# Optimization experiments

Measured on AMD Instinct MI355X. Metric: run time of the kernel, lower is better.

## Reference

```python
import jax, jax.numpy as jnp
import numpy as np
from jax import lax

BN_EPS = 1e-5
C = 256


def _conv_bn_relu(x, w, gamma, beta, mean, var):
    # x: [B,C,H,W], w: [C,C,3,3]; VALID conv, stride 1, then inference BN + ReLU
    y = lax.conv_general_dilated(x, w, window_strides=(1, 1), padding='VALID',
                                 dimension_numbers=('NCHW', 'OIHW', 'NCHW'))
    scale = gamma * lax.rsqrt(var + BN_EPS)
    shift = beta - mean * scale
    y = y * scale[None, :, None, None] + shift[None, :, None, None]
    return jax.nn.relu(y)


def _xcorr_depthwise(search, kernel):
    # search: [B,C,Hs,Ws], kernel: [B,C,Hk,Wk]
    # per-(batch, channel) valid cross-correlation (groups = B*C in torch)
    c = search.shape[1]

    def one(s, k):  # s: [C,Hs,Ws], k: [C,Hk,Wk]
        return lax.conv_general_dilated(
            s[None], k[:, None], window_strides=(1, 1), padding='VALID',
            dimension_numbers=('NCHW', 'OIHW', 'NCHW'),
            feature_group_count=c)[0]

    return jax.vmap(one)(search, kernel)  # [B,C,Ho,Wo]


def setup_inputs() -> dict:
    key = jax.random.key(0)
    ks = jax.random.split(key, 8)
    B = 128
    kernel = jax.random.normal(ks[0], (B, C, 7, 7), dtype=jnp.float32)
    search = jax.random.normal(ks[1], (B, C, 31, 31), dtype=jnp.float32)
    std = np.sqrt(2.0 / (3 * 3 * C)).astype(np.float32)
    w_kernel = jax.random.normal(ks[2], (C, C, 3, 3), dtype=jnp.float32) * std
    w_search = jax.random.normal(ks[3], (C, C, 3, 3), dtype=jnp.float32) * std
    bn_k_gamma = jnp.ones((C,), jnp.float32)
    bn_k_beta = jnp.zeros((C,), jnp.float32)
    bn_k_mean = jax.random.normal(ks[4], (C,), dtype=jnp.float32) * 0.1
    bn_k_var = jax.random.uniform(ks[5], (C,), dtype=jnp.float32, minval=0.5, maxval=1.5)
    bn_s_gamma = jnp.ones((C,), jnp.float32)
    bn_s_beta = jnp.zeros((C,), jnp.float32)
    bn_s_mean = jax.random.normal(ks[6], (C,), dtype=jnp.float32) * 0.1
    bn_s_var = jax.random.uniform(ks[7], (C,), dtype=jnp.float32, minval=0.5, maxval=1.5)
    return dict(kernel=kernel, search=search,
                w_kernel=w_kernel, bn_k_gamma=bn_k_gamma, bn_k_beta=bn_k_beta,
                bn_k_mean=bn_k_mean, bn_k_var=bn_k_var,
                w_search=w_search, bn_s_gamma=bn_s_gamma, bn_s_beta=bn_s_beta,
                bn_s_mean=bn_s_mean, bn_s_var=bn_s_var)


def reference(kernel, search, w_kernel, bn_k_gamma, bn_k_beta, bn_k_mean, bn_k_var,
              w_search, bn_s_gamma, bn_s_beta, bn_s_mean, bn_s_var):
    k = _conv_bn_relu(kernel, w_kernel, bn_k_gamma, bn_k_beta, bn_k_mean, bn_k_var)  # [B,C,5,5]
    s = _conv_bn_relu(search, w_search, bn_s_gamma, bn_s_beta, bn_s_mean, bn_s_var)  # [B,C,29,29]
    return _xcorr_depthwise(s, k)  # [B,C,25,25]
```

## Files before the change

### kernel.cpp

```cpp
#include <hip/hip_runtime.h>
#include <hip/hip_bf16.h>

#define BN_EPS 1e-5f
constexpr int C = 256;

typedef __attribute__((ext_vector_type(8))) short bf16x8;
typedef __attribute__((ext_vector_type(4))) float f32x4;

static __device__ __forceinline__ unsigned short f2bf(float f) {
    __hip_bfloat16 h = __float2bfloat16(f);
    return *reinterpret_cast<unsigned short*>(&h);
}
static __device__ __forceinline__ float bf2f(unsigned short u) {
    unsigned int v = ((unsigned int)u) << 16;
    return __uint_as_float(v);
}
static __device__ __forceinline__ unsigned int pack_bf2(float a, float b) {
    return (unsigned int)f2bf(a) | ((unsigned int)f2bf(b) << 16);
}

__global__ __launch_bounds__(256) void wprep_both(
    const float* __restrict__ wk, const float* __restrict__ bkg, const float* __restrict__ bkv,
    unsigned short* __restrict__ wkt,
    const float* __restrict__ ws, const float* __restrict__ bsg, const float* __restrict__ bsv,
    unsigned short* __restrict__ wst)
{
    const int bid = blockIdx.x, t = threadIdx.x;
    const bool isk = bid < 256;
    const int n = isk ? bid : bid - 256;
    const float* w = isk ? wk : ws;
    const float* g = isk ? bkg : bsg;
    const float* v = isk ? bkv : bsv;
    unsigned short* wt = isk ? wkt : wst;
    const float scale = g[n] * rsqrtf(v[n] + BN_EPS);
    const float* wp = w + ((size_t)n * C + t) * 9;
#pragma unroll
    for (int k = 0; k < 9; ++k)
        wt[((size_t)k * C + n) * C + t] = f2bf(wp[k] * scale);
}

__global__ __launch_bounds__(512, 2) void mega_conv(
    const float* __restrict__ sin_,
    const float* __restrict__ kin,
    const unsigned short* __restrict__ wst,
    const unsigned short* __restrict__ wkt,
    const float* __restrict__ bsg, const float* __restrict__ bsb,
    const float* __restrict__ bsm, const float* __restrict__ bsv,
    const float* __restrict__ bkg, const float* __restrict__ bkb,
    const float* __restrict__ bkm, const float* __restrict__ bkv,
    unsigned short* __restrict__ sbuf,
    float* __restrict__ kbuf)
{
    constexpr int WOUT = 29, NPOS = 841;
    constexpr int BM = 224, MF = 7, NF = 4;
    constexpr int LDK = 36;
    constexpr int ROWS = 11;
    constexpr int APIX = ROWS * 31;
    constexpr int ABUF = APIX * LDK;
    constexpr int BBUF = 256 * LDK;
    constexpr int BIT = 2;

    __shared__ __align__(16) short s_a[2 * ABUF];
    __shared__ __align__(16) short s_b[4 * BBUF];

    const int bid = blockIdx.x;
    const int t = threadIdx.x;
    const int lane = t & 63, wave = t >> 6;
    const int lr = lane >> 4, lc = lane & 15;

    if (bid >= 512) {
        constexpr int KW = 7, KHW = 49, KWOUT = 5, KNPOS = 25;
        constexpr int KMF = 2, KNF = 2;
        const int kb = bid - 512;
        const int n0 = (kb & 1) * 128;
        const int b0 = (kb >> 1) * 2;
        const int wm = wave >> 2, wn = wave & 3;

        short* ka = s_a;

        int arow[KMF];
#pragma unroll
        for (int m = 0; m < KMF; ++m) {
            int p = m * 16 + lc;
            p = p < KNPOS ? p : KNPOS - 1;
            int y = p / KWOUT, x = p - y * KWOUT;
            arow[m] = ((wm * KHW) + y * KW + x) * LDK + lr * 8;
        }

        f32x4 acc[KMF][KNF];
#pragma unroll
        for (int m = 0; m < KMF; ++m)
#pragma unroll
            for (int n = 0; n < KNF; ++n) acc[m][n] = f32x4{0.f, 0.f, 0.f, 0.f};

        const bool kval = lane < KHW;
        int sbb[4], scq[4];
#pragma unroll
        for (int j = 0; j < 4; ++j) {
            int idx = wave * 4 + j;
            sbb[j] = idx >> 4; scq[j] = (idx & 15) * 2;
        }
        const float* kbase = kin + (size_t)b0 * C * KHW + lane;

        float k0s[4], k1s[4];
#define KA_LOAD(c0_)                                                           \
        _Pragma("unroll")                                                      \
        for (int j = 0; j < 4; ++j) {                                          \
            if (kval) {                                                        \
                const float* p_ = kbase + ((size_t)sbb[j] * C + (c0_) + scq[j]) * KHW; \
                k0s[j] = p_[0]; k1s[j] = p_[KHW];                              \
            }                                                                  \
        }
#define KA_WRITE()                                                             \
        _Pragma("unroll")                                                      \
        for (int j = 0; j < 4; ++j) {                                          \
            if (kval)                                                          \
                *(unsigned int*)&ka[(sbb[j] * KHW + lane) * LDK + scq[j]] =    \
                    pack_bf2(k0s[j], k1s[j]);                                  \
        }

        const unsigned short* wb = wkt + (size_t)(n0 + wn * 32 + lc) * C + lr * 8;

        KA_LOAD(0)
        KA_WRITE()

#pragma unroll 1
        for (int ch = 0; ch < 8; ++ch) {
            const int c0 = ch * 32;
            __syncthreads();

            if (ch < 7) { KA_LOAD(c0 + 32) }

            bf16x8 bcur[KNF], bnxt[KNF];
#pragma unroll
            for (int n = 0; n < KNF; ++n)
                bnxt[n] = *(const bf16x8*)&wb[(size_t)0 + n * (16 * C) + c0];

#pragma unroll
            for (int tap = 0; tap < 9; ++tap) {
                const int dy = tap / 3, dx = tap % 3;
#pragma unroll
                for (int n = 0; n < KNF; ++n) bcur[n] = bnxt[n];
                if (tap < 8) {
#pragma unroll
                    for (int n = 0; n < KNF; ++n)
                        bnxt[n] = *(const bf16x8*)&wb[(size_t)(tap + 1) * (C * C) + n * (16 * C) + c0];
                }
                bf16x8 af[KMF];
#pragma unroll
                for (int m = 0; m < KMF; ++m)
                    af[m] = *(const bf16x8*)&ka[arow[m] + (dy * KW + dx) * LDK];
#pragma unroll
                for (int m = 0; m < KMF; ++m)
#pragma unroll
                    for (int n = 0; n < KNF; ++n)
                        acc[m][n] = __builtin_amdgcn_mfma_f32_16x16x32_bf16(
                            af[m], bcur[n], acc[m][n], 0, 0, 0);
            }

            __syncthreads();
            if (ch < 7) { KA_WRITE() }
        }
#undef KA_LOAD
#undef KA_WRITE

#pragma unroll
        for (int n = 0; n < KNF; ++n) {
            const int co = n0 + wn * 32 + n * 16 + lc;
            const float sc = bkg[co] * rsqrtf(bkv[co] + BN_EPS);
            const float bias = bkb[co] - bkm[co] * sc;
#pragma unroll
            for (int m = 0; m < KMF; ++m) {
                int p = m * 16 + lr * 4;
                int b = b0 + wm;
                f32x4 v = acc[m][n];
                float rr[4] = {fmaxf(v.x + bias, 0.f), fmaxf(v.y + bias, 0.f),
                               fmaxf(v.z + bias, 0.f), fmaxf(v.w + bias, 0.f)};
                float* op = kbuf + ((size_t)b * C + co) * 28 + p;
#pragma unroll
                for (int i = 0; i < 4; ++i)
                    if (p + i < KNPOS) op[i] = rr[i];
            }
        }
        return;
    }

    const int wm = wave >> 2, wn = wave & 3;
    const int p0 = (bid & 3) * BM;
    const int b  = bid >> 2;
    const int y0 = p0 / WOUT;
    const int R  = min(ROWS, 31 - y0);
    const int npix = R * 31;

    int arow[MF];
#pragma unroll
    for (int m = 0; m < MF; ++m) {
        int pm = wm * 112 + m * 16 + lc;
        int p = p0 + pm; p = p < NPOS ? p : NPOS - 1;
        int y = p / WOUT, x = p - y * WOUT;
        arow[m] = ((y - y0) * 31 + x) * LDK + lr * 8;
    }

    const float* abase = sin_ + (size_t)b * C * 961 + y0 * 31 + lane;
    bool segv[6];
    int dstq[2];
#pragma unroll
    for (int seg = 0; seg < 6; ++seg) segv[seg] = (seg * 64 + lane) < npix;
#pragma unroll
    for (int q = 0; q < 2; ++q) dstq[q] = 2 * (wave + q * 8);

    float a0s[12], a1s[12];
#define SA_LOAD(c0_)                                                           \
    _Pragma("unroll")                                                          \
    for (int q = 0; q < 2; ++q) {                                              \
        const size_t cq_ = (size_t)((c0_) + dstq[q]) * 961;                    \
        _Pragma("unroll")                                                      \
        for (int seg = 0; seg < 6; ++seg) {                                    \
            if (segv[seg]) {                                                   \
                a0s[q * 6 + seg] = abase[cq_ + seg * 64];                      \
                a1s[q * 6 + seg] = abase[cq_ + 961 + seg * 64];                \
            }                                                                  \
        }                                                                      \
    }
#define SA_WRITE(dst_)                                                         \
    _Pragma("unroll")                                                          \
    for (int q = 0; q < 2; ++q) {                                              \
        _Pragma("unroll")                                                      \
        for (int seg = 0; seg < 6; ++seg) {                                    \
            if (segv[seg])                                                     \
                *(unsigned int*)&s_a[(dst_) + (seg * 64 + lane) * LDK + dstq[q]] = \
                    pack_bf2(a0s[q * 6 + seg], a1s[q * 6 + seg]);              \
        }                                                                      \
    }

    const unsigned short* bptr[BIT]; int boff[BIT];
#pragma unroll
    for (int it = 0; it < BIT; ++it) {
        int i = t + it * 512;
        int n = i >> 2, sl = i & 3;
        bptr[it] = wst + (size_t)n * 256 + sl * 8;
        boff[it] = n * LDK + sl * 8;
    }

    f32x4 acc[MF][NF];
#pragma unroll
    for (int m = 0; m < MF; ++m)
#pragma unroll
        for (int n = 0; n < NF; ++n) acc[m][n] = f32x4{0.f, 0.f, 0.f, 0.f};

    bf16x8 bstg0[BIT], bstg1[BIT];

    SA_LOAD(0)
#pragma unroll
    for (int it = 0; it < BIT; ++it) bstg0[it] = *(const bf16x8*)(bptr[it]);
#pragma unroll
    for (int it = 0; it < BIT; ++it) bstg1[it] = *(const bf16x8*)(bptr[it] + 65536);
    SA_WRITE(0)
#pragma unroll
    for (int it = 0; it < BIT; ++it) *(bf16x8*)&s_b[boff[it]] = bstg0[it];
#pragma unroll
    for (int it = 0; it < BIT; ++it) *(bf16x8*)&s_b[BBUF + boff[it]] = bstg1[it];
    __syncthreads();

#define READ_FRAGS(S, AF, BF)                                                  \
    {                                                                          \
        const int tap_ = (S) % 9;                                              \
        const int dt_ = (tap_ / 3) * 31 + (tap_ % 3);                          \
        const int ab_ = (((S) / 9) & 1) * ABUF;                                \
        const int bb_ = ((S) & 3) * BBUF;                                      \
        _Pragma("unroll")                                                      \
        for (int n = 0; n < NF; ++n)                                           \
            BF[n] = *(const bf16x8*)&s_b[bb_ + (wn * 64 + n * 16 + lc) * LDK + lr * 8]; \
        _Pragma("unroll")                                                      \
        for (int m = 0; m < MF; ++m)                                           \
            AF[m] = *(const bf16x8*)&s_a[ab_ + arow[m] + dt_ * LDK];           \
    }

#define MFMA_STEP(AF, BF)                                                      \
    _Pragma("unroll")                                                          \
    for (int m = 0; m < MF; ++m)                                               \
        _Pragma("unroll")                                                      \
        for (int n = 0; n < NF; ++n)                                           \
            acc[m][n] = __builtin_amdgcn_mfma_f32_16x16x32_bf16(               \
                AF[m], BF[n], acc[m][n], 0, 0, 0);

#pragma unroll 1
    for (int pr = 0; pr < 35; ++pr) {
        const int s0 = 2 * pr, s1 = s0 + 1;

        {
            const int cb = (s0 % 9 == 0) ? s0 / 9 : ((s1 % 9 == 0) ? s1 / 9 : -1);
            if (cb >= 0 && cb < 7) {
                const int cn = (cb + 1) * 32;
                SA_LOAD(cn)
            }
        }

        bf16x8 af0[MF], bf0[NF], af1[MF], bf1[NF];
        READ_FRAGS(s0, af0, bf0)
        READ_FRAGS(s1, af1, bf1)

        MFMA_STEP(af0, bf0)

        {
            const int u0 = s0 + 2, u1 = s1 + 2;
            const int t0 = u0 % 9, c0_ = (u0 / 9) * 32;
            const int t1 = u1 % 9, c1_ = (u1 / 9) * 32;
#pragma unroll
            for (int it = 0; it < BIT; ++it)
                bstg0[it] = *(const bf16x8*)(bptr[it] + (size_t)t0 * 65536 + c0_);
#pragma unroll
            for (int it = 0; it < BIT; ++it)
                bstg1[it] = *(const bf16x8*)(bptr[it] + (size_t)t1 * 65536 + c1_);
        }

        MFMA_STEP(af1, bf1)

        {
            const int w0 = ((s0 + 2) & 3) * BBUF, w1 = ((s1 + 2) & 3) * BBUF;
#pragma unroll
            for (int it = 0; it < BIT; ++it)
                *(bf16x8*)&s_b[w0 + boff[it]] = bstg0[it];
#pragma unroll
            for (int it = 0; it < BIT; ++it)
                *(bf16x8*)&s_b[w1 + boff[it]] = bstg1[it];
        }

        {
            const int cw = (s0 % 9 == 7) ? s0 / 9 : ((s1 % 9 == 7) ? s1 / 9 : -1);
            if (cw >= 0 && cw < 7) {
                const int dst = ((cw & 1) ^ 1) * ABUF;
                SA_WRITE(dst)
            }
        }
        __syncthreads();
    }

    {
        bf16x8 af0[MF], bf0[NF], af1[MF], bf1[NF];
        READ_FRAGS(70, af0, bf0)
        READ_FRAGS(71, af1, bf1)
        MFMA_STEP(af0, bf0)
        MFMA_STEP(af1, bf1)
    }
#undef READ_FRAGS
#undef MFMA_STEP
#undef SA_LOAD
#undef SA_WRITE

#pragma unroll
    for (int n = 0; n < NF; ++n) {
        const int co = wn * 64 + n * 16 + lc;
        const float sc = bsg[co] * rsqrtf(bsv[co] + BN_EPS);
        const float bias = bsb[co] - bsm[co] * sc;
#pragma unroll
        for (int m = 0; m < MF; ++m) {
            int pm = wm * 112 + m * 16 + lr * 4;
            int p = p0 + pm;
            f32x4 v = acc[m][n];
            float r0 = fmaxf(v.x + bias, 0.f);
            float r1 = fmaxf(v.y + bias, 0.f);
            float r2 = fmaxf(v.z + bias, 0.f);
            float r3 = fmaxf(v.w + bias, 0.f);
            unsigned short* op = sbuf + ((size_t)b * C + co) * 844 + p;
            if (p + 4 <= NPOS) {
                ushort4 pk;
                pk.x = f2bf(r0); pk.y = f2bf(r1); pk.z = f2bf(r2); pk.w = f2bf(r3);
                *(ushort4*)op = pk;
            } else {
                float rr[4] = {r0, r1, r2, r3};
#pragma unroll
                for (int i = 0; i < 4; ++i)
                    if (p + i < NPOS) op[i] = f2bf(rr[i]);
            }
        }
    }
}

__global__ __launch_bounds__(256) void xcorr_dw(
    const unsigned short* __restrict__ s, const float* __restrict__ k,
    float* __restrict__ out)
{
    const int bc0 = blockIdx.x * 2;
    const int t = threadIdx.x;

    __shared__ float s_s[2][844];
    __shared__ float s_k[2][25];

#pragma unroll
    for (int it = 0; it < 2; ++it) {
        int i = t + it * 256;
        if (i < 422) {
            int pl = i < 211 ? 0 : 1;
            int q = i - pl * 211;
            ushort4 v = *(const ushort4*)(s + (size_t)(bc0 + pl) * 844 + 4 * q);
            s_s[pl][4 * q + 0] = bf2f(v.x);
            s_s[pl][4 * q + 1] = bf2f(v.y);
            s_s[pl][4 * q + 2] = bf2f(v.z);
            s_s[pl][4 * q + 3] = bf2f(v.w);
        }
    }
    if (t < 50) s_k[t / 25][t % 25] = k[(size_t)(bc0 + t / 25) * 28 + t % 25];
    __syncthreads();

    if (t >= 250) return;
    const int ch = t / 125;
    const int r = t - ch * 125;
    const int y = r / 5;
    const int xb = (r - y * 5) * 5;

    float kk[25];
#pragma unroll
    for (int i = 0; i < 25; ++i) kk[i] = s_k[ch][i];

    float w[5][9];
#pragma unroll
    for (int dy = 0; dy < 5; ++dy)
#pragma unroll
        for (int dx = 0; dx < 9; ++dx)
            w[dy][dx] = s_s[ch][(y + dy) * 29 + xb + dx];

    float o[5] = {0.f, 0.f, 0.f, 0.f, 0.f};
#pragma unroll
    for (int dy = 0; dy < 5; ++dy)
#pragma unroll
        for (int dx = 0; dx < 5; ++dx) {
            const float kv = kk[dy * 5 + dx];
#pragma unroll
            for (int oo = 0; oo < 5; ++oo)
                o[oo] += w[dy][oo + dx] * kv;
        }

    float* op = out + (size_t)(bc0 + ch) * 625 + y * 25 + xb;
#pragma unroll
    for (int oo = 0; oo < 5; ++oo) op[oo] = o[oo];
}

extern "C" void kernel_launch(void* const* d_in, const int* in_sizes, int n_in,
                              void* d_out, int out_size, void* d_ws, size_t ws_size,
                              hipStream_t stream) {
    const float* kin = (const float*)d_in[0];
    const float* sin_ = (const float*)d_in[1];
    const float* wk = (const float*)d_in[2];
    const float* bkg = (const float*)d_in[3];
    const float* bkb = (const float*)d_in[4];
    const float* bkm = (const float*)d_in[5];
    const float* bkv = (const float*)d_in[6];
    const float* ws_ = (const float*)d_in[7];
    const float* bsg = (const float*)d_in[8];
    const float* bsb = (const float*)d_in[9];
    const float* bsm = (const float*)d_in[10];
    const float* bsv = (const float*)d_in[11];
    float* out = (float*)d_out;

    char* base = (char*)d_ws;
    unsigned short* wkt = (unsigned short*)base;
    unsigned short* wst = wkt + (size_t)9 * C * C;
    unsigned short* sbuf = (unsigned short*)(base + 2359296);
    float* kbuf = (float*)(base + 2359296 + 55312384);

    wprep_both<<<512, 256, 0, stream>>>(wk, bkg, bkv, wkt, ws_, bsg, bsv, wst);

    mega_conv<<<640, 512, 0, stream>>>(
        sin_, kin, wst, wkt,
        bsg, bsb, bsm, bsv, bkg, bkb, bkm, bkv,
        sbuf, kbuf);

    xcorr_dw<<<128 * (C / 2), 256, 0, stream>>>(sbuf, kbuf, out);
}
```

Measured before the change: 224.2 us.

## Make conv kernel persistent: 256 blocks each run two search tiles plus a kernel tile

```diff
diff --git a/kernel.cpp b/kernel.cpp
--- a/kernel.cpp
+++ b/kernel.cpp
@@ -63,18 +63,212 @@
     __shared__ __align__(16) short s_a[2 * ABUF];
     __shared__ __align__(16) short s_b[4 * BBUF];
 
-    const int bid = blockIdx.x;
     const int t = threadIdx.x;
     const int lane = t & 63, wave = t >> 6;
     const int lr = lane >> 4, lc = lane & 15;
-
-    if (bid >= 512) {
+    const int wm = wave >> 2, wn = wave & 3;
+
+#pragma unroll 1
+    for (int sit = 0; sit < 2; ++sit) {
+        const int sid = blockIdx.x + sit * 256;
+        const int p0 = (sid & 3) * BM;
+        const int b  = sid >> 2;
+        const int y0 = p0 / WOUT;
+        const int R  = min(ROWS, 31 - y0);
+        const int npix = R * 31;
+
+        int arow[MF];
+#pragma unroll
+        for (int m = 0; m < MF; ++m) {
+            int pm = wm * 112 + m * 16 + lc;
+            int p = p0 + pm; p = p < NPOS ? p : NPOS - 1;
+            int y = p / WOUT, x = p - y * WOUT;
+            arow[m] = ((y - y0) * 31 + x) * LDK + lr * 8;
+        }
+
+        const float* abase = sin_ + (size_t)b * C * 961 + y0 * 31 + lane;
+        bool segv[6];
+        int dstq[2];
+#pragma unroll
+        for (int seg = 0; seg < 6; ++seg) segv[seg] = (seg * 64 + lane) < npix;
+#pragma unroll
+        for (int q = 0; q < 2; ++q) dstq[q] = 2 * (wave + q * 8);
+
+        float a0s[12], a1s[12];
+#define SA_LOAD(c0_)                                                           \
+        _Pragma("unroll")                                                      \
+        for (int q = 0; q < 2; ++q) {                                          \
+            const size_t cq_ = (size_t)((c0_) + dstq[q]) * 961;                \
+            _Pragma("unroll")                                                  \
+            for (int seg = 0; seg < 6; ++seg) {                                \
+                if (segv[seg]) {                                               \
+                    a0s[q * 6 + seg] = abase[cq_ + seg * 64];                  \
+                    a1s[q * 6 + seg] = abase[cq_ + 961 + seg * 64];            \
+                }                                                              \
+            }                                                                  \
+        }
+#define SA_WRITE(dst_)                                                         \
+        _Pragma("unroll")                                                      \
+        for (int q = 0; q < 2; ++q) {                                          \
+            _Pragma("unroll")                                                  \
+            for (int seg = 0; seg < 6; ++seg) {                                \
+                if (segv[seg])                                                 \
+                    *(unsigned int*)&s_a[(dst_) + (seg * 64 + lane) * LDK + dstq[q]] = \
+                        pack_bf2(a0s[q * 6 + seg], a1s[q * 6 + seg]);          \
+            }                                                                  \
+        }
+
+        const unsigned short* bptr[BIT]; int boff[BIT];
+#pragma unroll
+        for (int it = 0; it < BIT; ++it) {
+            int i = t + it * 512;
+            int n = i >> 2, sl = i & 3;
+            bptr[it] = wst + (size_t)n * 256 + sl * 8;
+            boff[it] = n * LDK + sl * 8;
+        }
+
+        f32x4 acc[MF][NF];
+#pragma unroll
+        for (int m = 0; m < MF; ++m)
+#pragma unroll
+            for (int n = 0; n < NF; ++n) acc[m][n] = f32x4{0.f, 0.f, 0.f, 0.f};
+
+        bf16x8 bstg0[BIT], bstg1[BIT];
+
+        SA_LOAD(0)
+#pragma unroll
+        for (int it = 0; it < BIT; ++it) bstg0[it] = *(const bf16x8*)(bptr[it]);
+#pragma unroll
+        for (int it = 0; it < BIT; ++it) bstg1[it] = *(const bf16x8*)(bptr[it] + 65536);
+        SA_WRITE(0)
+#pragma unroll
+        for (int it = 0; it < BIT; ++it) *(bf16x8*)&s_b[boff[it]] = bstg0[it];
+#pragma unroll
+        for (int it = 0; it < BIT; ++it) *(bf16x8*)&s_b[BBUF + boff[it]] = bstg1[it];
+        __syncthreads();
+
+#define READ_FRAGS(S, AF, BF)                                                  \
+        {                                                                      \
+            const int tap_ = (S) % 9;                                          \
+            const int dt_ = (tap_ / 3) * 31 + (tap_ % 3);                      \
+            const int ab_ = (((S) / 9) & 1) * ABUF;                            \
+            const int bb_ = ((S) & 3) * BBUF;                                  \
+            _Pragma("unroll")                                                  \
+            for (int n = 0; n < NF; ++n)                                       \
+                BF[n] = *(const bf16x8*)&s_b[bb_ + (wn * 64 + n * 16 + lc) * LDK + lr * 8]; \
+            _Pragma("unroll")                                                  \
+            for (int m = 0; m < MF; ++m)                                       \
+                AF[m] = *(const bf16x8*)&s_a[ab_ + arow[m] + dt_ * LDK];       \
+        }
+
+#define MFMA_STEP(AF, BF)                                                      \
+        _Pragma("unroll")                                                      \
+        for (int m = 0; m < MF; ++m)                                           \
+            _Pragma("unroll")                                                  \
+            for (int n = 0; n < NF; ++n)                                       \
+                acc[m][n] = __builtin_amdgcn_mfma_f32_16x16x32_bf16(           \
+                    AF[m], BF[n], acc[m][n], 0, 0, 0);
+
+#pragma unroll 1
+        for (int pr = 0; pr < 35; ++pr) {
+            const int s0 = 2 * pr, s1 = s0 + 1;
+
+            {
+                const int cb = (s0 % 9 == 0) ? s0 / 9 : ((s1 % 9 == 0) ? s1 / 9 : -1);
+                if (cb >= 0 && cb < 7) {
+                    const int cn = (cb + 1) * 32;
+                    SA_LOAD(cn)
+                }
+            }
+
+            bf16x8 af0[MF], bf0[NF], af1[MF], bf1[NF];
+            READ_FRAGS(s0, af0, bf0)
+            READ_FRAGS(s1, af1, bf1)
+
+            MFMA_STEP(af0, bf0)
+
+            {
+                const int u0 = s0 + 2, u1 = s1 + 2;
+                const int t0 = u0 % 9, c0_ = (u0 / 9) * 32;
+                const int t1 = u1 % 9, c1_ = (u1 / 9) * 32;
+#pragma unroll
+                for (int it = 0; it < BIT; ++it)
+                    bstg0[it] = *(const bf16x8*)(bptr[it] + (size_t)t0 * 65536 + c0_);
+#pragma unroll
+                for (int it = 0; it < BIT; ++it)
+                    bstg1[it] = *(const bf16x8*)(bptr[it] + (size_t)t1 * 65536 + c1_);
+            }
+
+            MFMA_STEP(af1, bf1)
+
+            {
+                const int w0 = ((s0 + 2) & 3) * BBUF, w1 = ((s1 + 2) & 3) * BBUF;
+#pragma unroll
+                for (int it = 0; it < BIT; ++it)
+                    *(bf16x8*)&s_b[w0 + boff[it]] = bstg0[it];
+#pragma unroll
+                for (int it = 0; it < BIT; ++it)
+                    *(bf16x8*)&s_b[w1 + boff[it]] = bstg1[it];
+            }
+
+            {
+                const int cw = (s0 % 9 == 7) ? s0 / 9 : ((s1 % 9 == 7) ? s1 / 9 : -1);
+                if (cw >= 0 && cw < 7) {
+                    const int dst = ((cw & 1) ^ 1) * ABUF;
+                    SA_WRITE(dst)
+                }
+            }
+            __syncthreads();
+        }
+
+        {
+            bf16x8 af0[MF], bf0[NF], af1[MF], bf1[NF];
+            READ_FRAGS(70, af0, bf0)
+            READ_FRAGS(71, af1, bf1)
+            MFMA_STEP(af0, bf0)
+            MFMA_STEP(af1, bf1)
+        }
+
+#pragma unroll
+        for (int n = 0; n < NF; ++n) {
+            const int co = wn * 64 + n * 16 + lc;
+            const float sc = bsg[co] * rsqrtf(bsv[co] + BN_EPS);
+            const float bias = bsb[co] - bsm[co] * sc;
+#pragma unroll
+            for (int m = 0; m < MF; ++m) {
+                int pm = wm * 112 + m * 16 + lr * 4;
+                int p = p0 + pm;
+                f32x4 v = acc[m][n];
+                float r0 = fmaxf(v.x + bias, 0.f);
+                float r1 = fmaxf(v.y + bias, 0.f);
+                float r2 = fmaxf(v.z + bias, 0.f);
+                float r3 = fmaxf(v.w + bias, 0.f);
+                unsigned short* op = sbuf + ((size_t)b * C + co) * 844 + p;
+                if (p + 4 <= NPOS) {
+                    ushort4 pk;
+                    pk.x = f2bf(r0); pk.y = f2bf(r1); pk.z = f2bf(r2); pk.w = f2bf(r3);
+                    *(ushort4*)op = pk;
+                } else {
+                    float rr[4] = {r0, r1, r2, r3};
+#pragma unroll
+                    for (int i = 0; i < 4; ++i)
+                        if (p + i < NPOS) op[i] = f2bf(rr[i]);
+                }
+            }
+        }
+        __syncthreads();
+#undef READ_FRAGS
+#undef MFMA_STEP
+#undef SA_LOAD
+#undef SA_WRITE
+    }
+
+    {
         constexpr int KW = 7, KHW = 49, KWOUT = 5, KNPOS = 25;
-        constexpr int KMF = 2, KNF = 2;
-        const int kb = bid - 512;
-        const int n0 = (kb & 1) * 128;
-        const int b0 = (kb >> 1) * 2;
-        const int wm = wave >> 2, wn = wave & 3;
+        constexpr int KMF = 2;
+        const int kb = blockIdx.x;
+        const int n0 = (kb & 3) * 64;
+        const int b0 = (kb >> 2) * 2;
 
         short* ka = s_a;
 
@@ -87,11 +281,9 @@
             arow[m] = ((wm * KHW) + y * KW + x) * LDK + lr * 8;
         }
 
-        f32x4 acc[KMF][KNF];
-#pragma unroll
-        for (int m = 0; m < KMF; ++m)
-#pragma unroll
-            for (int n = 0; n < KNF; ++n) acc[m][n] = f32x4{0.f, 0.f, 0.f, 0.f};
+        f32x4 acc[KMF];
+#pragma unroll
+        for (int m = 0; m < KMF; ++m) acc[m] = f32x4{0.f, 0.f, 0.f, 0.f};
 
         const bool kval = lane < KHW;
         int sbb[4], scq[4];
@@ -119,7 +311,7 @@
                     pack_bf2(k0s[j], k1s[j]);                                  \
         }
 
-        const unsigned short* wb = wkt + (size_t)(n0 + wn * 32 + lc) * C + lr * 8;
+        const unsigned short* wb = wkt + (size_t)(n0 + wn * 16 + lc) * C + lr * 8;
 
         KA_LOAD(0)
         KA_WRITE()
@@ -131,31 +323,23 @@
 
             if (ch < 7) { KA_LOAD(c0 + 32) }
 
-            bf16x8 bcur[KNF], bnxt[KNF];
-#pragma unroll
-            for (int n = 0; n < KNF; ++n)
-                bnxt[n] = *(const bf16x8*)&wb[(size_t)0 + n * (16 * C) + c0];
+            bf16x8 bcur, bnxt;
+            bnxt = *(const bf16x8*)&wb[c0];
 
 #pragma unroll
             for (int tap = 0; tap < 9; ++tap) {
                 const int dy = tap / 3, dx = tap % 3;
-#pragma unroll
-                for (int n = 0; n < KNF; ++n) bcur[n] = bnxt[n];
-                if (tap < 8) {
-#pragma unroll
-                    for (int n = 0; n < KNF; ++n)
-                        bnxt[n] = *(const bf16x8*)&wb[(size_t)(tap + 1) * (C * C) + n * (16 * C) + c0];
-                }
+                bcur = bnxt;
+                if (tap < 8)
+                    bnxt = *(const bf16x8*)&wb[(size_t)(tap + 1) * (C * C) + c0];
                 bf16x8 af[KMF];
 #pragma unroll
                 for (int m = 0; m < KMF; ++m)
                     af[m] = *(const bf16x8*)&ka[arow[m] + (dy * KW + dx) * LDK];
 #pragma unroll
                 for (int m = 0; m < KMF; ++m)
-#pragma unroll
-                    for (int n = 0; n < KNF; ++n)
-                        acc[m][n] = __builtin_amdgcn_mfma_f32_16x16x32_bf16(
-                            af[m], bcur[n], acc[m][n], 0, 0, 0);
+                    acc[m] = __builtin_amdgcn_mfma_f32_16x16x32_bf16(
+                        af[m], bcur, acc[m], 0, 0, 0);
             }
 
             __syncthreads();
@@ -164,214 +348,21 @@
 #undef KA_LOAD
 #undef KA_WRITE
 
-#pragma unroll
-        for (int n = 0; n < KNF; ++n) {
-            const int co = n0 + wn * 32 + n * 16 + lc;
+        {
+            const int co = n0 + wn * 16 + lc;
             const float sc = bkg[co] * rsqrtf(bkv[co] + BN_EPS);
             const float bias = bkb[co] - bkm[co] * sc;
 #pragma unroll
             for (int m = 0; m < KMF; ++m) {
                 int p = m * 16 + lr * 4;
                 int b = b0 + wm;
-                f32x4 v = acc[m][n];
+                f32x4 v = acc[m];
                 float rr[4] = {fmaxf(v.x + bias, 0.f), fmaxf(v.y + bias, 0.f),
                                fmaxf(v.z + bias, 0.f), fmaxf(v.w + bias, 0.f)};
                 float* op = kbuf + ((size_t)b * C + co) * 28 + p;
 #pragma unroll
                 for (int i = 0; i < 4; ++i)
                     if (p + i < KNPOS) op[i] = rr[i];
-            }
-        }
-        return;
-    }
-
-    const int wm = wave >> 2, wn = wave & 3;
-    const int p0 = (bid & 3) * BM;
-    const int b  = bid >> 2;
-    const int y0 = p0 / WOUT;
-    const int R  = min(ROWS, 31 - y0);
-    const int npix = R * 31;
-
-    int arow[MF];
-#pragma unroll
-    for (int m = 0; m < MF; ++m) {
-        int pm = wm * 112 + m * 16 + lc;
-        int p = p0 + pm; p = p < NPOS ? p : NPOS - 1;
-        int y = p / WOUT, x = p - y * WOUT;
-        arow[m] = ((y - y0) * 31 + x) * LDK + lr * 8;
-    }
-
-    const float* abase = sin_ + (size_t)b * C * 961 + y0 * 31 + lane;
-    bool segv[6];
-    int dstq[2];
-#pragma unroll
-    for (int seg = 0; seg < 6; ++seg) segv[seg] = (seg * 64 + lane) < npix;
-#pragma unroll
-    for (int q = 0; q < 2; ++q) dstq[q] = 2 * (wave + q * 8);
-
-    float a0s[12], a1s[12];
-#define SA_LOAD(c0_)                                                           \
-    _Pragma("unroll")                                                          \
-    for (int q = 0; q < 2; ++q) {                                              \
-        const size_t cq_ = (size_t)((c0_) + dstq[q]) * 961;                    \
-        _Pragma("unroll")                                                      \
-        for (int seg = 0; seg < 6; ++seg) {                                    \
-            if (segv[seg]) {                                                   \
-                a0s[q * 6 + seg] = abase[cq_ + seg * 64];                      \
-                a1s[q * 6 + seg] = abase[cq_ + 961 + seg * 64];                \
-            }                                                                  \
-        }                                                                      \
-    }
-#define SA_WRITE(dst_)                                                         \
-    _Pragma("unroll")                                                          \
-    for (int q = 0; q < 2; ++q) {                                              \
-        _Pragma("unroll")                                                      \
-        for (int seg = 0; seg < 6; ++seg) {                                    \
-            if (segv[seg])                                                     \
-                *(unsigned int*)&s_a[(dst_) + (seg * 64 + lane) * LDK + dstq[q]] = \
-                    pack_bf2(a0s[q * 6 + seg], a1s[q * 6 + seg]);              \
-        }                                                                      \
-    }
-
-    const unsigned short* bptr[BIT]; int boff[BIT];
-#pragma unroll
-    for (int it = 0; it < BIT; ++it) {
-        int i = t + it * 512;
-        int n = i >> 2, sl = i & 3;
-        bptr[it] = wst + (size_t)n * 256 + sl * 8;
-        boff[it] = n * LDK + sl * 8;
-    }
-
-    f32x4 acc[MF][NF];
-#pragma unroll
-    for (int m = 0; m < MF; ++m)
-#pragma unroll
-        for (int n = 0; n < NF; ++n) acc[m][n] = f32x4{0.f, 0.f, 0.f, 0.f};
-
-    bf16x8 bstg0[BIT], bstg1[BIT];
-
-    SA_LOAD(0)
-#pragma unroll
-    for (int it = 0; it < BIT; ++it) bstg0[it] = *(const bf16x8*)(bptr[it]);
-#pragma unroll
-    for (int it = 0; it < BIT; ++it) bstg1[it] = *(const bf16x8*)(bptr[it] + 65536);
-    SA_WRITE(0)
-#pragma unroll
-    for (int it = 0; it < BIT; ++it) *(bf16x8*)&s_b[boff[it]] = bstg0[it];
-#pragma unroll
-    for (int it = 0; it < BIT; ++it) *(bf16x8*)&s_b[BBUF + boff[it]] = bstg1[it];
-    __syncthreads();
-
-#define READ_FRAGS(S, AF, BF)                                                  \
-    {                                                                          \
-        const int tap_ = (S) % 9;                                              \
-        const int dt_ = (tap_ / 3) * 31 + (tap_ % 3);                          \
-        const int ab_ = (((S) / 9) & 1) * ABUF;                                \
-        const int bb_ = ((S) & 3) * BBUF;                                      \
-        _Pragma("unroll")                                                      \
-        for (int n = 0; n < NF; ++n)                                           \
-            BF[n] = *(const bf16x8*)&s_b[bb_ + (wn * 64 + n * 16 + lc) * LDK + lr * 8]; \
-        _Pragma("unroll")                                                      \
-        for (int m = 0; m < MF; ++m)                                           \
-            AF[m] = *(const bf16x8*)&s_a[ab_ + arow[m] + dt_ * LDK];           \
-    }
-
-#define MFMA_STEP(AF, BF)                                                      \
-    _Pragma("unroll")                                                          \
-    for (int m = 0; m < MF; ++m)                                               \
-        _Pragma("unroll")                                                      \
-        for (int n = 0; n < NF; ++n)                                           \
-            acc[m][n] = __builtin_amdgcn_mfma_f32_16x16x32_bf16(               \
-                AF[m], BF[n], acc[m][n], 0, 0, 0);
-
-#pragma unroll 1
-    for (int pr = 0; pr < 35; ++pr) {
-        const int s0 = 2 * pr, s1 = s0 + 1;
-
-        {
-            const int cb = (s0 % 9 == 0) ? s0 / 9 : ((s1 % 9 == 0) ? s1 / 9 : -1);
-            if (cb >= 0 && cb < 7) {
-                const int cn = (cb + 1) * 32;
-                SA_LOAD(cn)
-            }
-        }
-
-        bf16x8 af0[MF], bf0[NF], af1[MF], bf1[NF];
-        READ_FRAGS(s0, af0, bf0)
-        READ_FRAGS(s1, af1, bf1)
-
-        MFMA_STEP(af0, bf0)
-
-        {
-            const int u0 = s0 + 2, u1 = s1 + 2;
-            const int t0 = u0 % 9, c0_ = (u0 / 9) * 32;
-            const int t1 = u1 % 9, c1_ = (u1 / 9) * 32;
-#pragma unroll
-            for (int it = 0; it < BIT; ++it)
-                bstg0[it] = *(const bf16x8*)(bptr[it] + (size_t)t0 * 65536 + c0_);
-#pragma unroll
-            for (int it = 0; it < BIT; ++it)
-                bstg1[it] = *(const bf16x8*)(bptr[it] + (size_t)t1 * 65536 + c1_);
-        }
-
-        MFMA_STEP(af1, bf1)
-
-        {
-            const int w0 = ((s0 + 2) & 3) * BBUF, w1 = ((s1 + 2) & 3) * BBUF;
-#pragma unroll
-            for (int it = 0; it < BIT; ++it)
-                *(bf16x8*)&s_b[w0 + boff[it]] = bstg0[it];
-#pragma unroll
-            for (int it = 0; it < BIT; ++it)
-                *(bf16x8*)&s_b[w1 + boff[it]] = bstg1[it];
-        }
-
-        {
-            const int cw = (s0 % 9 == 7) ? s0 / 9 : ((s1 % 9 == 7) ? s1 / 9 : -1);
-            if (cw >= 0 && cw < 7) {
-                const int dst = ((cw & 1) ^ 1) * ABUF;
-                SA_WRITE(dst)
-            }
-        }
-        __syncthreads();
-    }
-
-    {
-        bf16x8 af0[MF], bf0[NF], af1[MF], bf1[NF];
-        READ_FRAGS(70, af0, bf0)
-        READ_FRAGS(71, af1, bf1)
-        MFMA_STEP(af0, bf0)
-        MFMA_STEP(af1, bf1)
-    }
-#undef READ_FRAGS
-#undef MFMA_STEP
-#undef SA_LOAD
-#undef SA_WRITE
-
-#pragma unroll
-    for (int n = 0; n < NF; ++n) {
-        const int co = wn * 64 + n * 16 + lc;
-        const float sc = bsg[co] * rsqrtf(bsv[co] + BN_EPS);
-        const float bias = bsb[co] - bsm[co] * sc;
-#pragma unroll
-        for (int m = 0; m < MF; ++m) {
-            int pm = wm * 112 + m * 16 + lr * 4;
-            int p = p0 + pm;
-            f32x4 v = acc[m][n];
-            float r0 = fmaxf(v.x + bias, 0.f);
-            float r1 = fmaxf(v.y + bias, 0.f);
-            float r2 = fmaxf(v.z + bias, 0.f);
-            float r3 = fmaxf(v.w + bias, 0.f);
-            unsigned short* op = sbuf + ((size_t)b * C + co) * 844 + p;
-            if (p + 4 <= NPOS) {
-                ushort4 pk;
-                pk.x = f2bf(r0); pk.y = f2bf(r1); pk.z = f2bf(r2); pk.w = f2bf(r3);
-                *(ushort4*)op = pk;
-            } else {
-                float rr[4] = {r0, r1, r2, r3};
-#pragma unroll
-                for (int i = 0; i < 4; ++i)
-                    if (p + i < NPOS) op[i] = f2bf(rr[i]);
             }
         }
     }
@@ -461,7 +452,7 @@
 
     wprep_both<<<512, 256, 0, stream>>>(wk, bkg, bkv, wkt, ws_, bsg, bsv, wst);
 
-    mega_conv<<<640, 512, 0, stream>>>(
+    mega_conv<<<256, 512, 0, stream>>>(
         sin_, kin, wst, wkt,
         bsg, bsb, bsm, bsv, bkg, bkb, bkm, bkv,
         sbuf, kbuf);
```

After: 227.4 us. No clear change (+1.5%).
